# Performance work log

Measured on AMD Instinct MI355X. Metric: run time of the kernel, lower is better.

The kernel has to match this reference:

```python
import jax, jax.numpy as jnp
import numpy as np

B, C, D, T = 64, 512, 32, 32
DT = D * T
K = 128            # valid_num: top-K proposals kept for NMS-style pooling
MARGIN = 0.2       # opt.global_margin
MAX_VIOLATION = True
EPS = 1e-8         # torch.cosine_similarity eps


def _l2n(x, axis):
    # torch cosine_similarity normalizes each vector by max(||x||, eps)
    return x / jnp.maximum(jnp.linalg.norm(x, axis=axis, keepdims=True), EPS)


def _cos(a, b, axis):
    return jnp.sum(_l2n(a, axis) * _l2n(b, axis), axis=axis)


def setup_inputs() -> dict:
    key = jax.random.key(0)
    k1, k2, k3 = jax.random.split(key, 3)
    videos = jax.random.normal(k1, (B, C, D, T), jnp.float32)
    sentences = jax.random.normal(k2, (B, C), jnp.float32)
    iou = jax.random.uniform(k3, (DT, DT), jnp.float32)
    iou_maps = 0.5 * (iou + iou.T)
    iou_maps = iou_maps.at[jnp.arange(DT), jnp.arange(DT)].set(1.0)
    mask = jnp.ones((D, T), jnp.float32)
    lam = jnp.asarray(0.125, jnp.float32)
    return {"videos": videos, "sentences": sentences, "lam": lam,
            "mask": mask, "valid_num": K, "iou_maps": iou_maps}


def reference(videos, sentences, lam, mask, valid_num, iou_maps):
    b, c, d, t = videos.shape
    dt = d * t
    # center over channel dim (dim=1 in torch)
    V = videos - jnp.mean(videos, axis=1, keepdims=True)          # [b,c,d,t]
    S = sentences - jnp.mean(sentences, axis=1, keepdims=True)    # [b,c]
    Vf = V.reshape(b, c, dt)
    Vn = _l2n(Vf, axis=1)                                         # unit over c
    Sn = _l2n(S, axis=1)
    mflat = mask.reshape(dt)

    # cosine sim of every sentence vs every video proposal: [b_sent, b_vid, dt]
    cross = jnp.einsum('ic,jcp->ijp', Sn, Vn)
    cross = jnp.where(mflat == 0, -jnp.inf, cross)

    # --- per-sample positive pooling (loop 1) ---
    self_score = cross[jnp.arange(b), jnp.arange(b)]              # [b, dt]
    w = jax.nn.softmax(self_score, axis=-1)
    video_pos = jnp.einsum('bp,bcp->bc', w, Vf)                   # [b, c]

    # sentence-sentence sims + hard negative mining
    sim = Sn @ Sn.T                                               # [b, b]
    idx = jnp.argsort(-sim, axis=1)                               # descending
    neg_idx = idx[:, 6:b - 5]                                     # b > 11 path
    neg_sents = S[neg_idx]                                        # [b, b-11, c]
    pos_score = _cos(video_pos, S, axis=1)                        # [b]
    neg_score = _cos(video_pos[:, None, :], neg_sents, axis=2)    # [b, b-11]
    vas_loss = jnp.mean(jax.nn.relu(MARGIN + neg_score - pos_score[:, None]), axis=1).mean()

    # cross-video pseudo-positive (crov), gated on nearest-neighbor sim > 0.9
    nn_idx = idx[:, 1]
    pse = Vf[nn_idx]                                              # [b, c, dt]
    vsim = jax.nn.softmax(_cos(video_pos[:, :, None], pse, axis=1), axis=-1)  # [b, dt]
    p_v = jnp.einsum('bp,bcp->bc', vsim, pse)
    n_v = jnp.einsum('bp,bcp->bc', (1.0 - vsim) * mflat, pse) / (valid_num - 1)
    crov = jax.nn.relu(MARGIN + _cos(video_pos, n_v, axis=1) - _cos(video_pos, p_v, axis=1))
    gate = sim[jnp.arange(b), nn_idx] > 0.9
    crov_loss = jnp.where(gate, crov, 0.0).mean()

    # --- NMS-weighted video score pooling (loop 2) ---
    pmap = self_score.reshape(b, d, t)                            # postive_map
    topv, topi = jax.lax.top_k(cross, valid_num)                  # [b,b,K]
    # pairwise IoU among the top-K proposals of each (sentence, video) pair
    iou = iou_maps[topi[..., :, None], topi[..., None, :]]        # [b,b,K,K]
    lower = jnp.tril(jnp.ones((valid_num, valid_num), bool), -1)  # l < k
    decay = jnp.prod(1.0 - jnp.where(lower, iou, 0.0), axis=-1)   # [b,b,K]
    wk = jax.nn.softmax(lam * topv, axis=-1)
    scores = jnp.sum(wk * decay * topv, axis=-1)                  # [b,b]

    # bidirectional margin ranking loss
    diag = jnp.diag(scores)[:, None]
    eye = jnp.eye(b, dtype=bool)
    cost_s = jnp.where(eye, 0.0, jax.nn.relu(MARGIN + scores - diag))
    cost_im = jnp.where(eye, 0.0, jax.nn.relu(MARGIN + scores - diag.T))
    if MAX_VIOLATION:
        cost_s = cost_s.max(axis=1)
        cost_im = cost_im.max(axis=0)
    loss = cost_s.sum() / b + cost_im.sum() / b + vas_loss + crov_loss
    return loss, pmap
```

## Files before the change

kernel.cpp:

```cpp
#include <hip/hip_runtime.h>
#include <hip/hip_fp16.h>
#include <math.h>

#define BB 64
#define CC 512
#define DTT 1024
#define NNEG 53
#define MARGIN_ 0.2f
#define EPSV 1e-8f

typedef short s16x8 __attribute__((ext_vector_type(8)));
typedef float f32x4 __attribute__((ext_vector_type(4)));

__device__ __forceinline__ float bred_sum(float v, float* red, int tid, int nt) {
  red[tid] = v; __syncthreads();
  for (int s = nt >> 1; s > 0; s >>= 1) { if (tid < s) red[tid] += red[tid + s]; __syncthreads(); }
  float r = red[0]; __syncthreads();
  return r;
}
__device__ __forceinline__ float bred_max(float v, float* red, int tid, int nt) {
  red[tid] = v; __syncthreads();
  for (int s = nt >> 1; s > 0; s >>= 1) { if (tid < s) red[tid] = fmaxf(red[tid], red[tid + s]); __syncthreads(); }
  float r = red[0]; __syncthreads();
  return r;
}

__global__ void k_sent(const float* __restrict__ sent, float* __restrict__ Sn,
                       float* __restrict__ SnT,
                       unsigned short* __restrict__ SnH, unsigned short* __restrict__ SnL,
                       float* __restrict__ SnSum) {
  int b = blockIdx.x, tid = threadIdx.x;
  __shared__ float red[256];
  float x0 = sent[b * CC + tid], x1 = sent[b * CC + tid + 256];
  float mean = bred_sum(x0 + x1, red, tid, 256) * (1.0f / CC);
  float s0 = x0 - mean, s1 = x1 - mean;
  float ss = bred_sum(s0 * s0 + s1 * s1, red, tid, 256);
  float nrm = fmaxf(sqrtf(ss), EPSV);
  float n0 = s0 / nrm, n1 = s1 / nrm;
  Sn[b * CC + tid] = n0; Sn[b * CC + tid + 256] = n1;
  SnT[tid * BB + b] = n0; SnT[(tid + 256) * BB + b] = n1;
  unsigned u0 = __float_as_uint(n0), u1 = __float_as_uint(n1);
  SnH[b * CC + tid] = (unsigned short)(u0 >> 16);
  SnH[b * CC + tid + 256] = (unsigned short)(u1 >> 16);
  float l0 = n0 - __uint_as_float(u0 & 0xFFFF0000u);
  float l1 = n1 - __uint_as_float(u1 & 0xFFFF0000u);
  SnL[b * CC + tid] = (unsigned short)(__float_as_uint(l0) >> 16);
  SnL[b * CC + tid + 256] = (unsigned short)(__float_as_uint(l1) >> 16);
  float sn = bred_sum(n0 + n1, red, tid, 256);
  if (tid == 0) SnSum[b] = sn;
}

__global__ void k_sim(const float* __restrict__ Sn, const float* __restrict__ SnT,
                      int* __restrict__ nn_idx, int* __restrict__ negidx,
                      float* __restrict__ nnsim) {
  int i = blockIdx.x, tid = threadIdx.x;
  int j = tid & 63, cq = tid >> 6;
  __shared__ float part[4][68];
  __shared__ float srow[BB];
  float acc = 0.f;
  const float* si = Sn + i * CC + cq * 128;
  const float* st = SnT + (size_t)(cq * 128) * BB + j;
#pragma unroll 8
  for (int c = 0; c < 128; ++c) acc = fmaf(si[c], st[(size_t)c * BB], acc);
  part[cq][j] = acc;
  __syncthreads();
  if (tid < 64) srow[tid] = part[0][tid] + part[1][tid] + part[2][tid] + part[3][tid];
  __syncthreads();
  if (tid < 64) {
    float mv = srow[tid];
    int rank = 0;
    for (int k = 0; k < BB; ++k) {
      float vk = srow[k];
      if (vk > mv || (vk == mv && k < tid)) rank++;
    }
    if (rank == 1) { nn_idx[i] = tid; nnsim[i] = mv; }
    if (rank >= 6 && rank < 59) negidx[i * NNEG + rank - 6] = tid;
  }
}

__global__ void k_prep_iou(const float* __restrict__ iou, __half* __restrict__ L16) {
  int g = (blockIdx.x * 256 + threadIdx.x) * 4;
  float4 x = *(const float4*)(iou + g);
  __half2 h0 = __floats2half2_rn(1.f - x.x, 1.f - x.y);
  __half2 h1 = __floats2half2_rn(1.f - x.z, 1.f - x.w);
  *(__half2*)(L16 + g) = h0;
  *(__half2*)(L16 + g + 2) = h1;
}

__global__ __launch_bounds__(64) void k_cross(const float* __restrict__ videos,
    const unsigned short* __restrict__ SnH, const unsigned short* __restrict__ SnL,
    const float* __restrict__ SnSum, const float* __restrict__ mask,
    float* __restrict__ cross, float* __restrict__ meanv, float* __restrict__ normv) {
  int lane = threadIdx.x;
  int bid = blockIdx.x;
  int j = bid >> 5;
  int pbase = (bid & 31) << 5;
  int row = lane & 15;
  int g = lane >> 4;
  int g8 = g << 3;

  const float* vbase = videos + (size_t)j * CC * DTT;

  f32x4 acc[4][2];
#pragma unroll
  for (int a = 0; a < 4; ++a)
#pragma unroll
    for (int pf = 0; pf < 2; ++pf)
#pragma unroll
      for (int r = 0; r < 4; ++r) acc[a][pf][r] = 0.f;

  float sac[2] = {0.f, 0.f}, ssac[2] = {0.f, 0.f};

#pragma unroll
  for (int t = 0; t < 16; ++t) {
    int kc = t * 32;
    s16x8 AH[4], AL[4];
#pragma unroll
    for (int a = 0; a < 4; ++a) {
      int off = (a * 16 + row) * CC + kc + g8;
      AH[a] = *(const s16x8*)(SnH + off);
      AL[a] = *(const s16x8*)(SnL + off);
    }
#pragma unroll
    for (int pf = 0; pf < 2; ++pf) {
      int p = pbase + pf * 16 + row;
      const float* bp = vbase + (size_t)(kc + g8) * DTT + p;
      float v[8];
#pragma unroll
      for (int q = 0; q < 8; ++q) v[q] = bp[(size_t)q * DTT];
      unsigned int hw[4], lw[4];
#pragma unroll
      for (int q = 0; q < 4; ++q) {
        float xe = v[2 * q], xo = v[2 * q + 1];
        unsigned ue = __float_as_uint(xe);
        unsigned uo = __float_as_uint(xo);
        hw[q] = (ue >> 16) | (uo & 0xFFFF0000u);
        float el = xe - __uint_as_float(ue & 0xFFFF0000u);
        float ol = xo - __uint_as_float(uo & 0xFFFF0000u);
        lw[q] = (__float_as_uint(el) >> 16) | (__float_as_uint(ol) & 0xFFFF0000u);
        sac[pf] += xe + xo;
        ssac[pf] = fmaf(xe, xe, ssac[pf]);
        ssac[pf] = fmaf(xo, xo, ssac[pf]);
      }
      union { unsigned int u[4]; s16x8 s; } bh, bl;
      bh.u[0] = hw[0]; bh.u[1] = hw[1]; bh.u[2] = hw[2]; bh.u[3] = hw[3];
      bl.u[0] = lw[0]; bl.u[1] = lw[1]; bl.u[2] = lw[2]; bl.u[3] = lw[3];
#pragma unroll
      for (int a = 0; a < 4; ++a) {
        acc[a][pf] = __builtin_amdgcn_mfma_f32_16x16x32_bf16(AH[a], bh.s, acc[a][pf], 0, 0, 0);
        acc[a][pf] = __builtin_amdgcn_mfma_f32_16x16x32_bf16(AH[a], bl.s, acc[a][pf], 0, 0, 0);
        acc[a][pf] = __builtin_amdgcn_mfma_f32_16x16x32_bf16(AL[a], bh.s, acc[a][pf], 0, 0, 0);
      }
    }
  }

  float sns[16];
#pragma unroll
  for (int a = 0; a < 4; ++a)
#pragma unroll
    for (int r = 0; r < 4; ++r) sns[a * 4 + r] = SnSum[a * 16 + (g << 2) + r];

#pragma unroll
  for (int pf = 0; pf < 2; ++pf) {
    float s = sac[pf], ss = ssac[pf];
    s += __shfl_xor(s, 16); s += __shfl_xor(s, 32);
    ss += __shfl_xor(ss, 16); ss += __shfl_xor(ss, 32);
    int p = pbase + pf * 16 + row;
    float mb = s * (1.0f / CC);
    float var = ss - s * mb;
    float nrm = fmaxf(sqrtf(fmaxf(var, 0.f)), EPSV);
    float inv = 1.f / nrm;
    if (g == 0) {
      meanv[j * DTT + p] = mb;
      normv[j * DTT + p] = nrm;
    }
    float mk = mask[p];
#pragma unroll
    for (int a = 0; a < 4; ++a) {
#pragma unroll
      for (int r = 0; r < 4; ++r) {
        int i = a * 16 + (g << 2) + r;
        float val = (acc[a][pf][r] - mb * sns[a * 4 + r]) * inv;
        if (mk == 0.f) val = -INFINITY;
        cross[((size_t)i * BB + j) * DTT + p] = val;
      }
    }
  }
}

__global__ void k_softmax_w(const float* __restrict__ cross, const float* __restrict__ meanv,
                            float* __restrict__ pmap, float* __restrict__ w, float* __restrict__ wm) {
  int b = blockIdx.x, tid = threadIdx.x;
  __shared__ float red[256];
  const float* row = cross + ((size_t)b * BB + b) * DTT;
  float v[4]; float mx = -INFINITY;
#pragma unroll
  for (int q = 0; q < 4; ++q) {
    v[q] = row[q * 256 + tid];
    pmap[b * DTT + q * 256 + tid] = v[q];
    mx = fmaxf(mx, v[q]);
  }
  mx = bred_max(mx, red, tid, 256);
  float e[4]; float se = 0.f;
#pragma unroll
  for (int q = 0; q < 4; ++q) { e[q] = expf(v[q] - mx); se += e[q]; }
  se = bred_sum(se, red, tid, 256);
  float inv = 1.f / se;
  float wmacc = 0.f;
#pragma unroll
  for (int q = 0; q < 4; ++q) {
    float wv = e[q] * inv;
    w[b * DTT + q * 256 + tid] = wv;
    wmacc += wv * meanv[b * DTT + q * 256 + tid];
  }
  wmacc = bred_sum(wmacc, red, tid, 256);
  if (tid == 0) wm[b] = wmacc;
}

__global__ void k_vpos(const float* __restrict__ videos, const float* __restrict__ w,
                       const float* __restrict__ wm, float* __restrict__ vp) {
  int wid = (blockIdx.x * 256 + threadIdx.x) >> 6;
  int lane = threadIdx.x & 63;
  int b = wid >> 9, c = wid & 511;
  const float4* vb = (const float4*)(videos + (size_t)(b * CC + c) * DTT) + lane * 4;
  const float4* wb = (const float4*)(w + b * DTT) + lane * 4;
  float acc = 0.f;
#pragma unroll
  for (int q = 0; q < 4; ++q) {
    float4 x = vb[q], y = wb[q];
    acc += x.x * y.x + x.y * y.y + x.z * y.z + x.w * y.w;
  }
#pragma unroll
  for (int off = 32; off > 0; off >>= 1) acc += __shfl_xor(acc, off);
  if (lane == 0) vp[b * CC + c] = acc - wm[b];
}

__global__ void k_vpnorm(const float* __restrict__ vp, float* __restrict__ vpn,
                         float* __restrict__ vpsum) {
  int b = blockIdx.x, tid = threadIdx.x;
  __shared__ float red[256];
  float x0 = vp[b * CC + tid], x1 = vp[b * CC + tid + 256];
  float ss = bred_sum(x0 * x0 + x1 * x1, red, tid, 256);
  float sm = bred_sum(x0 + x1, red, tid, 256);
  if (tid == 0) { vpn[b] = fmaxf(sqrtf(ss), EPSV); vpsum[b] = sm; }
}

__global__ void k_vsim_logits(const float* __restrict__ videos, const float* __restrict__ vp,
    const float* __restrict__ vpn, const float* __restrict__ vpsum, const int* __restrict__ nn_idx,
    const float* __restrict__ meanv, const float* __restrict__ normv, float* __restrict__ vslog) {
  int gid = blockIdx.x * 256 + threadIdx.x;
  int b = gid >> 10, p = gid & 1023;
  int nn = nn_idx[b];
  const float* base = videos + (size_t)nn * CC * DTT + p;
  const float* vpr = vp + b * CC;
  float acc = 0.f;
#pragma unroll 1
  for (int c0 = 0; c0 < CC; c0 += 16) {
    float v[16];
#pragma unroll
    for (int u = 0; u < 16; ++u) v[u] = base[(size_t)(c0 + u) * DTT];
#pragma unroll
    for (int u = 0; u < 16; ++u) acc = fmaf(vpr[c0 + u], v[u], acc);
  }
  acc -= meanv[nn * DTT + p] * vpsum[b];
  vslog[gid] = acc / (vpn[b] * normv[nn * DTT + p]);
}

__global__ void k_softmax_vsim(float* __restrict__ vslog, const int* __restrict__ nn_idx,
    const float* __restrict__ meanv, const float* __restrict__ mask,
    float* __restrict__ svp, float* __restrict__ svn) {
  int b = blockIdx.x, tid = threadIdx.x;
  __shared__ float red[256];
  int nn = nn_idx[b];
  float v[4]; float mx = -INFINITY;
#pragma unroll
  for (int q = 0; q < 4; ++q) { v[q] = vslog[b * DTT + q * 256 + tid]; mx = fmaxf(mx, v[q]); }
  mx = bred_max(mx, red, tid, 256);
  float e[4]; float se = 0.f;
#pragma unroll
  for (int q = 0; q < 4; ++q) { e[q] = expf(v[q] - mx); se += e[q]; }
  se = bred_sum(se, red, tid, 256);
  float inv = 1.f / se;
  float sp = 0.f, sn2 = 0.f;
#pragma unroll
  for (int q = 0; q < 4; ++q) {
    int p = q * 256 + tid;
    float vs = e[q] * inv;
    vslog[b * DTT + p] = vs;
    float mm = meanv[nn * DTT + p];
    sp += vs * mm;
    sn2 += (1.f - vs) * mask[p] * mm;
  }
  sp = bred_sum(sp, red, tid, 256);
  sn2 = bred_sum(sn2, red, tid, 256);
  if (tid == 0) { svp[b] = sp; svn[b] = sn2; }
}

__global__ void k_pvnv(const float* __restrict__ videos, const float* __restrict__ vsim,
    const int* __restrict__ nn_idx, const float* __restrict__ mask,
    const float* __restrict__ svp, const float* __restrict__ svn, const int* __restrict__ vn_p,
    float* __restrict__ pv, float* __restrict__ nv) {
  int wid = (blockIdx.x * 256 + threadIdx.x) >> 6;
  int lane = threadIdx.x & 63;
  int b = wid >> 9, c = wid & 511;
  int nn = nn_idx[b];
  const float4* vb = (const float4*)(videos + (size_t)(nn * CC + c) * DTT) + lane * 4;
  const float4* vs4 = (const float4*)(vsim + b * DTT) + lane * 4;
  const float4* m4 = ((const float4*)mask) + lane * 4;
  float ap = 0.f, an = 0.f;
#pragma unroll
  for (int q = 0; q < 4; ++q) {
    float4 x = vb[q], s = vs4[q], m = m4[q];
    ap += x.x * s.x + x.y * s.y + x.z * s.z + x.w * s.w;
    an += x.x * (1.f - s.x) * m.x + x.y * (1.f - s.y) * m.y + x.z * (1.f - s.z) * m.z + x.w * (1.f - s.w) * m.w;
  }
#pragma unroll
  for (int off = 32; off > 0; off >>= 1) { ap += __shfl_xor(ap, off); an += __shfl_xor(an, off); }
  if (lane == 0) {
    float kd = (float)(*vn_p - 1);
    pv[b * CC + c] = ap - svp[b];
    nv[b * CC + c] = (an - svn[b]) / kd;
  }
}

__global__ void k_vas(const float* __restrict__ vp, const float* __restrict__ vpn,
                      const float* __restrict__ SnT, const int* __restrict__ negidx,
                      float* __restrict__ vasrow) {
  int i = blockIdx.x, tid = threadIdx.x;
  int t = tid & 63, cq = tid >> 6;
  __shared__ float part[4][68];
  __shared__ float redv[64];
  __shared__ float red[256];
  int nj = (t < NNEG) ? negidx[i * NNEG + t] : i;
  float acc = 0.f;
  const float* vpr = vp + i * CC + cq * 128;
  const float* st = SnT + (size_t)(cq * 128) * BB + nj;
#pragma unroll 8
  for (int c = 0; c < 128; ++c) acc = fmaf(vpr[c], st[(size_t)c * BB], acc);
  part[cq][t] = acc;
  __syncthreads();
  if (tid < 64) redv[tid] = part[0][tid] + part[1][tid] + part[2][tid] + part[3][tid];
  __syncthreads();
  float invn = 1.f / vpn[i];
  float pos = redv[63] * invn;
  float contrib = (tid < NNEG) ? fmaxf(MARGIN_ + redv[tid] * invn - pos, 0.f) : 0.f;
  float s = bred_sum(contrib, red, tid, 256);
  if (tid == 0) vasrow[i] = s / (float)NNEG;
}

__global__ void k_crov(const float* __restrict__ vp, const float* __restrict__ vpn,
                       const float* __restrict__ pv, const float* __restrict__ nv,
                       const float* __restrict__ nnsim, float* __restrict__ crovrow) {
  int b = blockIdx.x, tid = threadIdx.x;
  __shared__ float red[256];
  float dp = 0.f, pp = 0.f, dn = 0.f, nn2 = 0.f;
  for (int c = tid; c < CC; c += 256) {
    float a = vp[b * CC + c], x = pv[b * CC + c], y = nv[b * CC + c];
    dp += a * x; pp += x * x; dn += a * y; nn2 += y * y;
  }
  dp = bred_sum(dp, red, tid, 256);
  pp = bred_sum(pp, red, tid, 256);
  dn = bred_sum(dn, red, tid, 256);
  nn2 = bred_sum(nn2, red, tid, 256);
  if (tid == 0) {
    float cosp = dp / (vpn[b] * fmaxf(sqrtf(pp), EPSV));
    float cosn = dn / (vpn[b] * fmaxf(sqrtf(nn2), EPSV));
    float crov = fmaxf(MARGIN_ + cosn - cosp, 0.f);
    crovrow[b] = (nnsim[b] > 0.9f) ? crov : 0.f;
  }
}

__global__ __launch_bounds__(256) void k_select(const float* __restrict__ cross,
    const int* __restrict__ vn_p, unsigned* __restrict__ ordi_g, float* __restrict__ ordv_g) {
  __shared__ unsigned int hist_s[4][256];
  __shared__ unsigned int sel_s[4][128];
  __shared__ unsigned int selk_s[4][128];
  __shared__ unsigned int cnt_s[4];
  int tid = threadIdx.x;
  int wv = tid >> 6, lane = tid & 63;
  int ij = blockIdx.x * 4 + wv;
  int K = *vn_p; if (K > 128) K = 128;
  unsigned int* hist = hist_s[wv];
  unsigned int* sel = sel_s[wv];
  unsigned int* selk = selk_s[wv];

  const float* row = cross + (size_t)ij * DTT;
  unsigned int v[16];
#pragma unroll
  for (int q = 0; q < 16; ++q) {
    unsigned u = __float_as_uint(row[q * 64 + lane]);
    v[q] = (u & 0x80000000u) ? ~u : (u | 0x80000000u);
  }
  if (lane == 0) cnt_s[wv] = 0u;
  __builtin_amdgcn_wave_barrier();

  unsigned prefix = 0u, pmask = 0u;
  int remaining = K;
  for (int shift = 24; shift >= 0; shift -= 8) {
#pragma unroll
    for (int q = 0; q < 4; ++q) hist[lane * 4 + q] = 0u;
    __builtin_amdgcn_wave_barrier();
#pragma unroll
    for (int q = 0; q < 16; ++q) {
      if ((v[q] & pmask) == prefix)
        atomicAdd(&hist[(v[q] >> shift) & 255u], 1u);
    }
    __builtin_amdgcn_wave_barrier();
    unsigned c0 = hist[lane * 4], c1 = hist[lane * 4 + 1];
    unsigned c2 = hist[lane * 4 + 2], c3 = hist[lane * 4 + 3];
    unsigned s = c0 + c1 + c2 + c3;
    unsigned inc = s;
#pragma unroll
    for (int off = 1; off < 64; off <<= 1) {
      unsigned t = __shfl_down(inc, off);
      if (lane + off < 64) inc += t;
    }
    unsigned exc = inc - s;
    bool found = (exc < (unsigned)remaining) && (inc >= (unsigned)remaining);
    unsigned long long bmask = __ballot(found);
    int winner = (int)(__ffsll((unsigned long long)bmask) - 1);
    unsigned packed = 0u;
    if (found) {
      unsigned c = exc;
      unsigned cc[4] = {c0, c1, c2, c3};
      int d = lane * 4;
#pragma unroll
      for (int q = 3; q >= 0; --q) {
        if (c + cc[q] >= (unsigned)remaining) { d = lane * 4 + q; break; }
        c += cc[q];
      }
      packed = ((unsigned)d << 16) | (unsigned)(remaining - (int)c);
    }
    packed = __shfl(packed, winner);
    prefix |= (packed >> 16) << shift;
    remaining = (int)(packed & 0xFFFFu);
    pmask |= 255u << shift;
  }

#pragma unroll
  for (int q = 0; q < 16; ++q) {
    if (v[q] > prefix) {
      unsigned pos = atomicAdd(&cnt_s[wv], 1u);
      sel[pos] = (unsigned)(q * 64 + lane);
      selk[pos] = v[q];
    }
  }
  __builtin_amdgcn_wave_barrier();
  {
    int base = K - remaining;
    int last = -1;
    for (int t = 0; t < remaining; ++t) {
      int mymin = 0x7FFFFFFF;
#pragma unroll
      for (int q = 0; q < 16; ++q) {
        int idx = q * 64 + lane;
        if (v[q] == prefix && idx > last && idx < mymin) mymin = idx;
      }
#pragma unroll
      for (int off = 32; off > 0; off >>= 1) mymin = min(mymin, __shfl_xor(mymin, off));
      if (lane == 0) { sel[base + t] = (unsigned)mymin; selk[base + t] = prefix; }
      last = mymin;
    }
  }
  __builtin_amdgcn_wave_barrier();

  for (int e = lane; e < K; e += 64) {
    unsigned myidx = sel[e], myk = selk[e];
    int rank = 0;
    for (int m = 0; m < K; ++m) {
      unsigned ok = selk[m];
      rank += (ok > myk || (ok == myk && sel[m] < myidx)) ? 1 : 0;
    }
    unsigned u = (myk & 0x80000000u) ? (myk & 0x7FFFFFFFu) : ~myk;
    ordi_g[ij * 128 + rank] = myidx;
    ordv_g[ij * 128 + rank] = __uint_as_float(u);
  }
}

__global__ __launch_bounds__(256) void k_decay(const __half* __restrict__ L16,
    const unsigned* __restrict__ ordi_g, const float* __restrict__ ordv_g,
    const float* __restrict__ lam_p, const int* __restrict__ vn_p,
    float* __restrict__ scores) {
  __shared__ unsigned ti[128];
  __shared__ float dks[128];
  int ij = blockIdx.x, tid = threadIdx.x;
  int wv = tid >> 6, lane = tid & 63;
  int K = *vn_p; if (K > 128) K = 128;
  float lam = *lam_p;
  if (tid < 128) {
    ti[tid] = (tid < K) ? ordi_g[ij * 128 + tid] : 0u;
    dks[tid] = 1.f;
  }
  __syncthreads();

  for (int r = wv; r < K; r += 4) {
    const __half* irow = L16 + (size_t)ti[r] * DTT;
    float f = 1.f;
    if (lane < r && lane < 64) f = __half2float(irow[ti[lane]]);
    float prod = f;
#pragma unroll
    for (int off = 32; off > 0; off >>= 1) prod *= __shfl_xor(prod, off);
    if (r > 64 && prod > 1e-14f) {
      float f2 = 1.f;
      int m = 64 + lane;
      if (m < r) f2 = __half2float(irow[ti[m]]);
#pragma unroll
      for (int off = 32; off > 0; off >>= 1) f2 *= __shfl_xor(f2, off);
      prod *= f2;
    }
    if (lane == 0) dks[r] = prod;
  }
  __syncthreads();

  if (wv == 0) {
    bool okA = (lane < K), okB = (lane + 64 < K);
    float vA = okA ? ordv_g[ij * 128 + lane] : 0.f;
    float vB = okB ? ordv_g[ij * 128 + lane + 64] : 0.f;
    float mx = fmaxf(okA ? lam * vA : -INFINITY, okB ? lam * vB : -INFINITY);
#pragma unroll
    for (int off = 32; off > 0; off >>= 1) mx = fmaxf(mx, __shfl_xor(mx, off));
    float eA = okA ? expf(lam * vA - mx) : 0.f;
    float eB = okB ? expf(lam * vB - mx) : 0.f;
    float se = eA + eB;
    float sc = (okA ? eA * dks[lane] * vA : 0.f) + (okB ? eB * dks[lane + 64] * vB : 0.f);
#pragma unroll
    for (int off = 32; off > 0; off >>= 1) {
      se += __shfl_xor(se, off);
      sc += __shfl_xor(sc, off);
    }
    if (lane == 0) scores[ij] = sc / se;
  }
}

__global__ void k_final(const float* __restrict__ scores, const float* __restrict__ vasrow,
                        const float* __restrict__ crovrow, float* __restrict__ out) {
  int tid = threadIdx.x;
  __shared__ float sm[BB * BB];
  __shared__ float red[64];
  for (int q = tid; q < BB * BB; q += 64) sm[q] = scores[q];
  __syncthreads();
  float di = sm[tid * BB + tid];
  float rowmax = 0.f, colmax = 0.f;
  for (int k = 0; k < BB; ++k) {
    if (k != tid) {
      rowmax = fmaxf(rowmax, fmaxf(MARGIN_ + sm[tid * BB + k] - di, 0.f));
      colmax = fmaxf(colmax, fmaxf(MARGIN_ + sm[k * BB + tid] - di, 0.f));
    }
  }
  float total = bred_sum(rowmax + colmax + vasrow[tid] + crovrow[tid], red, tid, 64);
  if (tid == 0) out[0] = total * (1.0f / BB);
}

extern "C" void kernel_launch(void* const* d_in, const int* in_sizes, int n_in,
                              void* d_out, int out_size, void* d_ws, size_t ws_size,
                              hipStream_t stream) {
  const float* videos = (const float*)d_in[0];
  const float* sentences = (const float*)d_in[1];
  const float* lam = (const float*)d_in[2];
  const float* mask = (const float*)d_in[3];
  const int* valid_num = (const int*)d_in[4];
  const float* iou_maps = (const float*)d_in[5];
  float* out = (float*)d_out;
  float* pmap = out + 1;

  float* ws = (float*)d_ws;
  float* Sn = ws;
  float* SnT = Sn + 32768;
  float* SnSum = SnT + 32768;
  float* meanv = SnSum + 64;
  float* normv = meanv + 65536;
  float* cross = normv + 65536;
  float* w = cross + 4194304;
  float* wm = w + 65536;
  float* vp = wm + 64;
  float* vpn = vp + 32768;
  float* vpsum = vpn + 64;
  float* nnsim = vpsum + 64;
  float* vslog = nnsim + 64;
  float* svp = vslog + 65536;
  float* svn = svp + 64;
  float* pvb = svn + 64;
  float* nvb = pvb + 32768;
  float* vasrow = nvb + 32768;
  float* crovrow = vasrow + 64;
  float* scores = crovrow + 64;
  int* nn_idx = (int*)(scores + 4096);
  int* negidx = nn_idx + 64;
  unsigned* ordi_g = (unsigned*)(negidx + 3392);
  float* ordv_g = (float*)(ordi_g + 524288);
  __half* L16 = (__half*)(ordv_g + 524288);
  unsigned short* SnH16 = (unsigned short*)(L16 + 1048576);
  unsigned short* SnL16 = SnH16 + 32768;

  k_sent<<<64, 256, 0, stream>>>(sentences, Sn, SnT, SnH16, SnL16, SnSum);
  k_sim<<<64, 256, 0, stream>>>(Sn, SnT, nn_idx, negidx, nnsim);
  k_prep_iou<<<1024, 256, 0, stream>>>(iou_maps, L16);
  k_cross<<<2048, 64, 0, stream>>>(videos, SnH16, SnL16, SnSum, mask, cross, meanv, normv);
  k_softmax_w<<<64, 256, 0, stream>>>(cross, meanv, pmap, w, wm);
  k_vpos<<<8192, 256, 0, stream>>>(videos, w, wm, vp);
  k_vpnorm<<<64, 256, 0, stream>>>(vp, vpn, vpsum);
  k_vsim_logits<<<256, 256, 0, stream>>>(videos, vp, vpn, vpsum, nn_idx, meanv, normv, vslog);
  k_softmax_vsim<<<64, 256, 0, stream>>>(vslog, nn_idx, meanv, mask, svp, svn);
  k_pvnv<<<8192, 256, 0, stream>>>(videos, vslog, nn_idx, mask, svp, svn, valid_num, pvb, nvb);
  k_vas<<<64, 256, 0, stream>>>(vp, vpn, SnT, negidx, vasrow);
  k_crov<<<64, 256, 0, stream>>>(vp, vpn, pvb, nvb, nnsim, crovrow);
  k_select<<<1024, 256, 0, stream>>>(cross, valid_num, ordi_g, ordv_g);
  k_decay<<<4096, 256, 0, stream>>>(L16, ordi_g, ordv_g, lam, valid_num, scores);
  k_final<<<1, 64, 0, stream>>>(scores, vasrow, crovrow, out);
}
```

Baseline: 435.8 us.

## Halve k_cross tile width and restructure k_decay via shared IoU tile

k_cross now gives each 64-thread block 16 proposal columns instead of 32 and launches twice as many blocks. This trades reuse of the sentence fragments for more parallelism and fewer live accumulators. k_decay no longer reduces each row with a wave-wide shuffle product. It gathers the lower-triangular IoU complement entries into a shared half-precision tile, then has one thread per row compute the product serially with split accumulators. The old early-exit that skipped the second half when the product was already tiny is gone, so more gathers always run.

```diff
diff --git a/kernel.cpp b/kernel.cpp
--- a/kernel.cpp
+++ b/kernel.cpp
@@ -93,23 +93,22 @@
     float* __restrict__ cross, float* __restrict__ meanv, float* __restrict__ normv) {
   int lane = threadIdx.x;
   int bid = blockIdx.x;
-  int j = bid >> 5;
-  int pbase = (bid & 31) << 5;
+  int j = bid >> 6;
+  int pbase = (bid & 63) << 4;
   int row = lane & 15;
   int g = lane >> 4;
   int g8 = g << 3;
 
   const float* vbase = videos + (size_t)j * CC * DTT;
 
-  f32x4 acc[4][2];
+  f32x4 acc[4];
 #pragma unroll
   for (int a = 0; a < 4; ++a)
 #pragma unroll
-    for (int pf = 0; pf < 2; ++pf)
-#pragma unroll
-      for (int r = 0; r < 4; ++r) acc[a][pf][r] = 0.f;
-
-  float sac[2] = {0.f, 0.f}, ssac[2] = {0.f, 0.f};
+    for (int r = 0; r < 4; ++r) acc[a][r] = 0.f;
+
+  float sac = 0.f, ssac = 0.f;
+  int p = pbase + row;
 
 #pragma unroll
   for (int t = 0; t < 16; ++t) {
@@ -121,36 +120,32 @@
       AH[a] = *(const s16x8*)(SnH + off);
       AL[a] = *(const s16x8*)(SnL + off);
     }
-#pragma unroll
-    for (int pf = 0; pf < 2; ++pf) {
-      int p = pbase + pf * 16 + row;
-      const float* bp = vbase + (size_t)(kc + g8) * DTT + p;
-      float v[8];
-#pragma unroll
-      for (int q = 0; q < 8; ++q) v[q] = bp[(size_t)q * DTT];
-      unsigned int hw[4], lw[4];
-#pragma unroll
-      for (int q = 0; q < 4; ++q) {
-        float xe = v[2 * q], xo = v[2 * q + 1];
-        unsigned ue = __float_as_uint(xe);
-        unsigned uo = __float_as_uint(xo);
-        hw[q] = (ue >> 16) | (uo & 0xFFFF0000u);
-        float el = xe - __uint_as_float(ue & 0xFFFF0000u);
-        float ol = xo - __uint_as_float(uo & 0xFFFF0000u);
-        lw[q] = (__float_as_uint(el) >> 16) | (__float_as_uint(ol) & 0xFFFF0000u);
-        sac[pf] += xe + xo;
-        ssac[pf] = fmaf(xe, xe, ssac[pf]);
-        ssac[pf] = fmaf(xo, xo, ssac[pf]);
-      }
-      union { unsigned int u[4]; s16x8 s; } bh, bl;
-      bh.u[0] = hw[0]; bh.u[1] = hw[1]; bh.u[2] = hw[2]; bh.u[3] = hw[3];
-      bl.u[0] = lw[0]; bl.u[1] = lw[1]; bl.u[2] = lw[2]; bl.u[3] = lw[3];
-#pragma unroll
-      for (int a = 0; a < 4; ++a) {
-        acc[a][pf] = __builtin_amdgcn_mfma_f32_16x16x32_bf16(AH[a], bh.s, acc[a][pf], 0, 0, 0);
-        acc[a][pf] = __builtin_amdgcn_mfma_f32_16x16x32_bf16(AH[a], bl.s, acc[a][pf], 0, 0, 0);
-        acc[a][pf] = __builtin_amdgcn_mfma_f32_16x16x32_bf16(AL[a], bh.s, acc[a][pf], 0, 0, 0);
-      }
+    const float* bp = vbase + (size_t)(kc + g8) * DTT + p;
+    float v[8];
+#pragma unroll
+    for (int q = 0; q < 8; ++q) v[q] = bp[(size_t)q * DTT];
+    unsigned int hw[4], lw[4];
+#pragma unroll
+    for (int q = 0; q < 4; ++q) {
+      float xe = v[2 * q], xo = v[2 * q + 1];
+      unsigned ue = __float_as_uint(xe);
+      unsigned uo = __float_as_uint(xo);
+      hw[q] = (ue >> 16) | (uo & 0xFFFF0000u);
+      float el = xe - __uint_as_float(ue & 0xFFFF0000u);
+      float ol = xo - __uint_as_float(uo & 0xFFFF0000u);
+      lw[q] = (__float_as_uint(el) >> 16) | (__float_as_uint(ol) & 0xFFFF0000u);
+      sac += xe + xo;
+      ssac = fmaf(xe, xe, ssac);
+      ssac = fmaf(xo, xo, ssac);
+    }
+    union { unsigned int u[4]; s16x8 s; } bh, bl;
+    bh.u[0] = hw[0]; bh.u[1] = hw[1]; bh.u[2] = hw[2]; bh.u[3] = hw[3];
+    bl.u[0] = lw[0]; bl.u[1] = lw[1]; bl.u[2] = lw[2]; bl.u[3] = lw[3];
+#pragma unroll
+    for (int a = 0; a < 4; ++a) {
+      acc[a] = __builtin_amdgcn_mfma_f32_16x16x32_bf16(AH[a], bh.s, acc[a], 0, 0, 0);
+      acc[a] = __builtin_amdgcn_mfma_f32_16x16x32_bf16(AH[a], bl.s, acc[a], 0, 0, 0);
+      acc[a] = __builtin_amdgcn_mfma_f32_16x16x32_bf16(AL[a], bh.s, acc[a], 0, 0, 0);
     }
   }
 
@@ -160,12 +155,10 @@
 #pragma unroll
     for (int r = 0; r < 4; ++r) sns[a * 4 + r] = SnSum[a * 16 + (g << 2) + r];
 
-#pragma unroll
-  for (int pf = 0; pf < 2; ++pf) {
-    float s = sac[pf], ss = ssac[pf];
+  {
+    float s = sac, ss = ssac;
     s += __shfl_xor(s, 16); s += __shfl_xor(s, 32);
     ss += __shfl_xor(ss, 16); ss += __shfl_xor(ss, 32);
-    int p = pbase + pf * 16 + row;
     float mb = s * (1.0f / CC);
     float var = ss - s * mb;
     float nrm = fmaxf(sqrtf(fmaxf(var, 0.f)), EPSV);
@@ -180,7 +173,7 @@
 #pragma unroll
       for (int r = 0; r < 4; ++r) {
         int i = a * 16 + (g << 2) + r;
-        float val = (acc[a][pf][r] - mb * sns[a * 4 + r]) * inv;
+        float val = (acc[a][r] - mb * sns[a * 4 + r]) * inv;
         if (mk == 0.f) val = -INFINITY;
         cross[((size_t)i * BB + j) * DTT + p] = val;
       }
@@ -482,33 +475,42 @@
     const float* __restrict__ lam_p, const int* __restrict__ vn_p,
     float* __restrict__ scores) {
   __shared__ unsigned ti[128];
+  __shared__ __half Lt[128][132];
   __shared__ float dks[128];
   int ij = blockIdx.x, tid = threadIdx.x;
   int wv = tid >> 6, lane = tid & 63;
   int K = *vn_p; if (K > 128) K = 128;
   float lam = *lam_p;
-  if (tid < 128) {
-    ti[tid] = (tid < K) ? ordi_g[ij * 128 + tid] : 0u;
-    dks[tid] = 1.f;
-  }
+  if (tid < 128) ti[tid] = (tid < K) ? ordi_g[ij * 128 + tid] : 0u;
   __syncthreads();
 
   for (int r = wv; r < K; r += 4) {
     const __half* irow = L16 + (size_t)ti[r] * DTT;
-    float f = 1.f;
-    if (lane < r && lane < 64) f = __half2float(irow[ti[lane]]);
-    float prod = f;
-#pragma unroll
-    for (int off = 32; off > 0; off >>= 1) prod *= __shfl_xor(prod, off);
-    if (r > 64 && prod > 1e-14f) {
-      float f2 = 1.f;
-      int m = 64 + lane;
-      if (m < r) f2 = __half2float(irow[ti[m]]);
-#pragma unroll
-      for (int off = 32; off > 0; off >>= 1) f2 *= __shfl_xor(f2, off);
-      prod *= f2;
-    }
-    if (lane == 0) dks[r] = prod;
+    if (lane < r) Lt[r][lane] = irow[ti[lane]];
+    int m = 64 + lane;
+    if (m < r) Lt[r][m] = irow[ti[m]];
+  }
+  __syncthreads();
+
+  if (tid < 128) {
+    float prod = 1.f;
+    if (tid < K && tid > 0) {
+      int r = tid;
+      const __half* rowp = &Lt[r][0];
+      float pa = 1.f, pb2 = 1.f;
+      int m = 0;
+      for (; m + 8 <= r; m += 8) {
+        float2 a = __half22float2(*(const __half2*)&rowp[m]);
+        float2 b = __half22float2(*(const __half2*)&rowp[m + 2]);
+        float2 c = __half22float2(*(const __half2*)&rowp[m + 4]);
+        float2 d = __half22float2(*(const __half2*)&rowp[m + 6]);
+        pa *= a.x * a.y; pb2 *= b.x * b.y;
+        pa *= c.x * c.y; pb2 *= d.x * d.y;
+      }
+      for (; m < r; ++m) pa *= __half2float(rowp[m]);
+      prod = pa * pb2;
+    }
+    dks[tid] = prod;
   }
   __syncthreads();
 
@@ -595,7 +597,7 @@
   k_sent<<<64, 256, 0, stream>>>(sentences, Sn, SnT, SnH16, SnL16, SnSum);
   k_sim<<<64, 256, 0, stream>>>(Sn, SnT, nn_idx, negidx, nnsim);
   k_prep_iou<<<1024, 256, 0, stream>>>(iou_maps, L16);
-  k_cross<<<2048, 64, 0, stream>>>(videos, SnH16, SnL16, SnSum, mask, cross, meanv, normv);
+  k_cross<<<4096, 64, 0, stream>>>(videos, SnH16, SnL16, SnSum, mask, cross, meanv, normv);
   k_softmax_w<<<64, 256, 0, stream>>>(cross, meanv, pmap, w, wm);
   k_vpos<<<8192, 256, 0, stream>>>(videos, w, wm, vp);
   k_vpnorm<<<64, 256, 0, stream>>>(vp, vpn, vpsum);
```

After: 472.9 us. 1.09x slower.
